# Optimization experiments

Hardware: AMD Instinct MI355X
Metric: run time of the kernel (lower is better)

## Reference

```python
import jax, jax.numpy as jnp
import numpy as np
import math

N_EMBD = 1024
N_HEADS = 16
B, T = 4, 2048

def setup_inputs() -> dict:
    key = jax.random.key(0)
    k1, k2, k3 = jax.random.split(key, 3)
    x = jax.random.normal(k1, (B, T, N_EMBD), dtype=jnp.float32)
    scale = 1.0 / math.sqrt(N_EMBD)
    W_attn = jax.random.normal(k2, (N_EMBD, 3 * N_EMBD), dtype=jnp.float32) * scale
    W_proj = jax.random.normal(k3, (N_EMBD, N_EMBD), dtype=jnp.float32) * scale
    return {"x": x, "W_attn": W_attn, "W_proj": W_proj}

def reference(x, W_attn, W_proj):
    Bb, Tt, C = x.shape
    hd = C // N_HEADS
    qkv = x @ W_attn  # [B,T,3C]
    q, k, v = jnp.split(qkv, 3, axis=-1)
    # [B,H,T,hd]
    q = q.reshape(Bb, Tt, N_HEADS, hd).transpose(0, 2, 1, 3)
    k = k.reshape(Bb, Tt, N_HEADS, hd).transpose(0, 2, 1, 3)
    v = v.reshape(Bb, Tt, N_HEADS, hd).transpose(0, 2, 1, 3)
    att = jnp.einsum('bhqd,bhkd->bhqk', q, k) * (1.0 / math.sqrt(hd))
    mask = jnp.tril(jnp.ones((Tt, Tt), dtype=bool))
    att = jnp.where(mask[None, None], att, -jnp.inf)
    att = jax.nn.softmax(att, axis=-1)
    out = jnp.einsum('bhqk,bhkd->bhqd', att, v)
    out = out.transpose(0, 2, 1, 3).reshape(Bb, Tt, C)
    return out @ W_proj
```

## Files before the change

kernel.cpp:

```cpp
#include <hip/hip_runtime.h>
#include <cstddef>
#include <cstdint>

typedef __attribute__((ext_vector_type(8))) _Float16 half8;
typedef __attribute__((ext_vector_type(4))) _Float16 half4;
typedef __attribute__((ext_vector_type(4))) float f32x4;
typedef __attribute__((ext_vector_type(16))) float f32x16;

#define N_EMBD 1024
#define N_HEADS 16
#define BATCH 4
#define SEQ 2048
#define C3 3072
#define HD 64

__device__ inline uint32_t pk2(float x, float y) {
    auto h2 = __builtin_amdgcn_cvt_pkrtz(x, y);
    uint32_t u;
    __builtin_memcpy(&u, &h2, 4);
    return u;
}

__device__ inline void swap32(uint32_t& a, uint32_t& b) {
    asm volatile("v_permlane32_swap_b32 %0, %1" : "+v"(a), "+v"(b));
}

__global__ void cvt_f32_f16(const float* __restrict__ in, _Float16* __restrict__ out, int n) {
    int i = (blockIdx.x * 256 + threadIdx.x) * 4;
    if (i >= n) return;
    float4 v = *(const float4*)(in + i);
    half4 h;
    h[0] = (_Float16)v.x; h[1] = (_Float16)v.y; h[2] = (_Float16)v.z; h[3] = (_Float16)v.w;
    *(half4*)(out + i) = h;
}

__global__ void transpose_cvt(const float* __restrict__ in, _Float16* __restrict__ out,
                              int R, int Ncols) {
    __shared__ float tile[32][33];
    int n0 = blockIdx.x * 32, r0 = blockIdx.y * 32;
    int tx = threadIdx.x, ty = threadIdx.y;
#pragma unroll
    for (int i = 0; i < 32; i += 8)
        tile[ty + i][tx] = in[(size_t)(r0 + ty + i) * Ncols + n0 + tx];
    __syncthreads();
#pragma unroll
    for (int i = 0; i < 32; i += 8)
        out[(size_t)(n0 + ty + i) * R + r0 + tx] = (_Float16)tile[tx][ty + i];
}

__global__ void transpose_v(const _Float16* __restrict__ qkv, _Float16* __restrict__ vT) {
    __shared__ _Float16 tile[32][36];
    int t0 = blockIdx.x * 32;
    int bhd = blockIdx.y;
    int bh = bhd >> 1, dh = bhd & 1;
    int b = bh >> 4, h = bh & 15;
    int tx = threadIdx.x, ty = threadIdx.y;
#pragma unroll
    for (int i = 0; i < 32; i += 8)
        tile[ty + i][tx] = qkv[(size_t)(b * SEQ + t0 + ty + i) * C3 + 2 * N_EMBD + h * HD + dh * 32 + tx];
    __syncthreads();
#pragma unroll
    for (int i = 0; i < 32; i += 8)
        vT[((size_t)bh * HD + dh * 32 + ty + i) * SEQ + t0 + tx] = tile[tx][ty + i];
}

__device__ inline void store1(float* p, float v) { *p = v; }
__device__ inline void store1(_Float16* p, float v) { *p = (_Float16)v; }

template <typename OutT>
__global__ __launch_bounds__(512, 1) void gemm192(
    const _Float16* __restrict__ A, const _Float16* __restrict__ Bt,
    OutT* __restrict__ C, int M, int N, int K) {
    __shared__ _Float16 Al[2][256 * 64];
    __shared__ _Float16 Bl[2][192 * 64];
    const int tid = threadIdx.x;
    const int lane = tid & 63, wave = tid >> 6;
    const int l15 = lane & 15, l4 = lane >> 4;
    const int wm = wave >> 2, wn = wave & 3;

    const int nwg = gridDim.x, nbx = N / 192;
    int wg = blockIdx.x;
    if ((nwg & 7) == 0) { int cpx = nwg >> 3; wg = (wg & 7) * cpx + (wg >> 3); }
    const int row0 = (wg / nbx) * 256, col0 = (wg % nbx) * 192;
    const int TAU = K >> 6;

    const int srow = tid >> 3, su = tid & 7;
    const int usrc8 = (su ^ (srow & 7)) * 8;
    auto stageAu = [&](int unit, int ts) {
        __builtin_amdgcn_global_load_lds(
            (const __attribute__((address_space(1))) void*)(A + (size_t)(row0 + unit * 64 + srow) * K + ts * 64 + usrc8),
            (__attribute__((address_space(3))) void*)(&Al[ts & 1][unit * 64 * 64 + tid * 8]), 16, 0, 0);
    };
    auto stageBu = [&](int unit, int ts) {
        __builtin_amdgcn_global_load_lds(
            (const __attribute__((address_space(1))) void*)(Bt + (size_t)(col0 + unit * 64 + srow) * K + ts * 64 + usrc8),
            (__attribute__((address_space(3))) void*)(&Bl[ts & 1][unit * 64 * 64 + tid * 8]), 16, 0, 0);
    };
    auto stageTile = [&](int ts) {
        stageAu(0, ts); stageAu(1, ts); stageAu(2, ts); stageAu(3, ts);
        stageBu(0, ts); stageBu(1, ts); stageBu(2, ts);
    };

    f32x4 acc[8][3] = {};
    stageTile(0); stageTile(1);
    asm volatile("s_waitcnt vmcnt(7)" ::: "memory");
    __builtin_amdgcn_s_barrier();

    half8 a[4][2], b[3][2];
    for (int tau = 0; tau < TAU; ++tau) {
        const _Float16* Ab = &Al[tau & 1][0];
        const _Float16* Bb = &Bl[tau & 1][0];
        const bool t2 = (tau + 2 < TAU);

#pragma unroll
        for (int m = 0; m < 4; ++m)
#pragma unroll
            for (int ks = 0; ks < 2; ++ks) {
                int r = wm * 128 + m * 16 + l15;
                a[m][ks] = *(const half8*)(Ab + r * 64 + (((ks * 4 + l4) ^ (r & 7)) * 8));
            }
#pragma unroll
        for (int n = 0; n < 3; ++n)
#pragma unroll
            for (int ks = 0; ks < 2; ++ks) {
                int r = wn * 48 + n * 16 + l15;
                b[n][ks] = *(const half8*)(Bb + r * 64 + (((ks * 4 + l4) ^ (r & 7)) * 8));
            }
        __builtin_amdgcn_s_barrier();
        __builtin_amdgcn_s_setprio(1);
#pragma unroll
        for (int m = 0; m < 4; ++m)
#pragma unroll
            for (int n = 0; n < 2; ++n)
#pragma unroll
                for (int ks = 0; ks < 2; ++ks)
                    acc[m][n] = __builtin_amdgcn_mfma_f32_16x16x32_f16(a[m][ks], b[n][ks], acc[m][n], 0, 0, 0);
        __builtin_amdgcn_s_setprio(0);
        __builtin_amdgcn_s_barrier();

        if (t2) { stageBu(0, tau + 2); stageBu(1, tau + 2); stageBu(2, tau + 2); }
        __builtin_amdgcn_s_barrier();
        __builtin_amdgcn_s_setprio(1);
#pragma unroll
        for (int m = 0; m < 4; ++m)
#pragma unroll
            for (int ks = 0; ks < 2; ++ks)
                acc[m][2] = __builtin_amdgcn_mfma_f32_16x16x32_f16(a[m][ks], b[2][ks], acc[m][2], 0, 0, 0);
        __builtin_amdgcn_s_setprio(0);
        __builtin_amdgcn_s_barrier();

#pragma unroll
        for (int m = 0; m < 4; ++m)
#pragma unroll
            for (int ks = 0; ks < 2; ++ks) {
                int r = wm * 128 + 64 + m * 16 + l15;
                a[m][ks] = *(const half8*)(Ab + r * 64 + (((ks * 4 + l4) ^ (r & 7)) * 8));
            }
        if (t2) { stageAu(0, tau + 2); stageAu(2, tau + 2); }
        __builtin_amdgcn_s_barrier();
        __builtin_amdgcn_s_setprio(1);
#pragma unroll
        for (int m = 0; m < 4; ++m)
#pragma unroll
            for (int n = 0; n < 2; ++n)
#pragma unroll
                for (int ks = 0; ks < 2; ++ks)
                    acc[4 + m][n] = __builtin_amdgcn_mfma_f32_16x16x32_f16(a[m][ks], b[n][ks], acc[4 + m][n], 0, 0, 0);
        __builtin_amdgcn_s_setprio(0);
        __builtin_amdgcn_s_barrier();

        if (t2) { stageAu(1, tau + 2); stageAu(3, tau + 2); }
        __builtin_amdgcn_s_barrier();
        __builtin_amdgcn_s_setprio(1);
#pragma unroll
        for (int m = 0; m < 4; ++m)
#pragma unroll
            for (int ks = 0; ks < 2; ++ks)
                acc[4 + m][2] = __builtin_amdgcn_mfma_f32_16x16x32_f16(a[m][ks], b[2][ks], acc[4 + m][2], 0, 0, 0);
        __builtin_amdgcn_s_setprio(0);
        if (tau <= TAU - 3) {
            asm volatile("s_waitcnt vmcnt(7)" ::: "memory");
        } else if (tau == TAU - 2) {
            asm volatile("s_waitcnt vmcnt(0)" ::: "memory");
        }
        __builtin_amdgcn_s_barrier();
    }

#pragma unroll
    for (int mi = 0; mi < 8; ++mi)
#pragma unroll
        for (int ni = 0; ni < 3; ++ni)
#pragma unroll
            for (int j = 0; j < 4; ++j) {
                int r = row0 + wm * 128 + (mi >> 2) * 64 + (mi & 3) * 16 + l4 * 4 + j;
                int c = col0 + wn * 48 + ni * 16 + l15;
                store1(C + (size_t)r * N + c, acc[mi][ni][j]);
            }
}

template <typename OutT>
__global__ __launch_bounds__(256, 2) void gemm_h(
    const _Float16* __restrict__ A, const _Float16* __restrict__ Bt,
    OutT* __restrict__ C, int M, int N, int K) {
    __shared__ _Float16 Al[3][128 * 32];
    __shared__ _Float16 Bl[3][128 * 32];
    const int tid = threadIdx.x;
    const int wave = tid >> 6, lane = tid & 63;
    const int l15 = lane & 15, l4 = lane >> 4;
    const int gx = gridDim.x;
    int lin = blockIdx.y * gx + blockIdx.x;
    int bcol, brow;
    if ((gx & 7) == 0) {
        int cpx = gx >> 3;
        int xcd = lin & 7;
        int idx = lin >> 3;
        bcol = xcd * cpx + idx % cpx;
        brow = idx / cpx;
    } else { bcol = blockIdx.x; brow = blockIdx.y; }
    const int row0 = brow * 128, col0 = bcol * 128;
    const int wm = wave >> 1, wn = wave & 1;
    const int TAU = K >> 5;

    auto stageT = [&](int ts, int buf) {
#pragma unroll
        for (int i = 0; i < 2; ++i) {
            int c = tid + 256 * i;
            int r = c >> 2, c8 = (c & 3) * 8;
            __builtin_amdgcn_global_load_lds(
                (const __attribute__((address_space(1))) void*)(A + (size_t)(row0 + r) * K + ts * 32 + c8),
                (__attribute__((address_space(3))) void*)(&Al[buf][(size_t)(wave * 64 + 256 * i) * 8]),
                16, 0, 0);
        }
#pragma unroll
        for (int i = 0; i < 2; ++i) {
            int c = tid + 256 * i;
            int r = c >> 2, c8 = (c & 3) * 8;
            __builtin_amdgcn_global_load_lds(
                (const __attribute__((address_space(1))) void*)(Bt + (size_t)(col0 + r) * K + ts * 32 + c8),
                (__attribute__((address_space(3))) void*)(&Bl[buf][(size_t)(wave * 64 + 256 * i) * 8]),
                16, 0, 0);
        }
    };

    f32x4 acc[4][4] = {};
    stageT(0, 0); stageT(1, 1);
    asm volatile("s_waitcnt vmcnt(4)" ::: "memory");
    __builtin_amdgcn_s_barrier();

    int cur = 0;
    for (int t = 0; t < TAU; ++t) {
        int sb = cur + 2; if (sb >= 3) sb -= 3;
        if (t + 2 < TAU) stageT(t + 2, sb);
        half8 a[4], b[4];
#pragma unroll
        for (int m = 0; m < 4; ++m)
            a[m] = *(const half8*)(&Al[cur][(wm * 64 + m * 16 + l15) * 32 + l4 * 8]);
#pragma unroll
        for (int n = 0; n < 4; ++n)
            b[n] = *(const half8*)(&Bl[cur][(wn * 64 + n * 16 + l15) * 32 + l4 * 8]);
        __builtin_amdgcn_s_setprio(1);
#pragma unroll
        for (int m = 0; m < 4; ++m)
#pragma unroll
            for (int n = 0; n < 4; ++n)
                acc[m][n] = __builtin_amdgcn_mfma_f32_16x16x32_f16(a[m], b[n], acc[m][n], 0, 0, 0);
        __builtin_amdgcn_s_setprio(0);
        if (t + 2 < TAU) {
            asm volatile("s_waitcnt vmcnt(4)" ::: "memory");
        } else if (t + 1 < TAU) {
            asm volatile("s_waitcnt vmcnt(0)" ::: "memory");
        }
        __builtin_amdgcn_s_barrier();
        ++cur; if (cur == 3) cur = 0;
    }
#pragma unroll
    for (int m = 0; m < 4; ++m)
#pragma unroll
        for (int n = 0; n < 4; ++n)
#pragma unroll
            for (int j = 0; j < 4; ++j) {
                int r = row0 + wm * 64 + m * 16 + l4 * 4 + j;
                int cc = col0 + wn * 64 + n * 16 + l15;
                store1(C + (size_t)r * N + cc, acc[m][n][j]);
            }
}

__global__ __launch_bounds__(256, 4) void attn_kernel(const _Float16* __restrict__ qkv,
                                                      const _Float16* __restrict__ vT,
                                                      _Float16* __restrict__ ao) {
    const int bid = blockIdx.x;
    const int qt = 15 - (bid >> 6);
    const int bh = bid & 63;
    const int b = bh >> 4, h = bh & 15;
    const int tid = threadIdx.x, lane = tid & 63;
    const int wave = tid >> 6;
    const int l31 = lane & 31, L = lane >> 5;

    __shared__ _Float16 Kl[2][64 * 64];
    __shared__ _Float16 Vl[2][64 * 64];

    const float qscale = 0.125f * 1.44269504089f;
    const float NEGC = -4.0f * 1.44269504089f;

    const int q0w = qt * 128 + wave * 32;
    const int q_g = q0w + l31;
    const int nt = 2 * qt + 2;

    auto stage = [&](int t, int buf) {
#pragma unroll
        for (int i = 0; i < 2; ++i) {
            int idx = tid + 256 * i;
            int key = idx >> 3, u = idx & 7;
            int d8 = (u ^ (key & 7)) * 8;
            __builtin_amdgcn_global_load_lds(
                (const __attribute__((address_space(1))) void*)(qkv + (size_t)(b * SEQ + t * 64 + key) * C3 + N_EMBD + h * HD + d8),
                (__attribute__((address_space(3))) void*)(&Kl[buf][idx * 8]), 16, 0, 0);
        }
#pragma unroll
        for (int i = 0; i < 2; ++i) {
            int idx = tid + 256 * i;
            int d = idx >> 3, u = idx & 7;
            int k8 = (u ^ (d & 7)) * 8;
            __builtin_amdgcn_global_load_lds(
                (const __attribute__((address_space(1))) void*)(vT + ((size_t)bh * HD + d) * SEQ + t * 64 + k8),
                (__attribute__((address_space(3))) void*)(&Vl[buf][idx * 8]), 16, 0, 0);
        }
    };

    stage(0, 0);

    half8 qb[4];
#pragma unroll
    for (int ks = 0; ks < 4; ++ks) {
        half8 v = *(const half8*)(qkv + (size_t)(b * SEQ + q_g) * C3 + h * HD + ks * 16 + L * 8);
#pragma unroll
        for (int e = 0; e < 8; ++e) v[e] = (_Float16)((float)v[e] * qscale);
        qb[ks] = v;
    }
    half8 onesf;
#pragma unroll
    for (int e = 0; e < 8; ++e) onesf[e] = (_Float16)1.0f;

    const f32x16 cinit = (f32x16)(NEGC);
    f32x16 o[2];
    o[0] = (f32x16)(0.f);
    o[1] = (f32x16)(0.f);
    f32x16 lac = (f32x16)(0.f);

    asm volatile("s_waitcnt vmcnt(0)" ::: "memory");
    __builtin_amdgcn_s_barrier();

    for (int t = 0; t < nt; ++t) {
        const int cur = t & 1;
        const int kv0 = t * 64;
        const bool pf = (t + 1 < nt);
        if (pf) stage(t + 1, cur ^ 1);

        if (kv0 <= q0w + 31) {
            const _Float16* Kb = &Kl[cur][0];
            const _Float16* Vb = &Vl[cur][0];
            f32x16 s[2];
            __builtin_amdgcn_s_setprio(1);
#pragma unroll
            for (int kb = 0; kb < 2; ++kb) {
                const int key = kb * 32 + l31;
                {
                    half8 kf = *(const half8*)(Kb + key * 64 + ((L ^ (key & 7)) * 8));
                    s[kb] = __builtin_amdgcn_mfma_f32_32x32x16_f16(kf, qb[0], cinit, 0, 0, 0);
                }
#pragma unroll
                for (int ks = 1; ks < 4; ++ks) {
                    half8 kf = *(const half8*)(Kb + key * 64 + (((ks * 2 + L) ^ (key & 7)) * 8));
                    s[kb] = __builtin_amdgcn_mfma_f32_32x32x16_f16(kf, qb[ks], s[kb], 0, 0, 0);
                }
            }
            __builtin_amdgcn_s_setprio(0);
            const bool needmask = (kv0 + 63 > q0w);
#pragma unroll
            for (int kb = 0; kb < 2; ++kb) {
#pragma unroll
                for (int r = 0; r < 16; ++r) {
                    float v = exp2f(s[kb][r]);
                    if (needmask) {
                        int key_g = kv0 + kb * 32 + (r & 3) + 8 * (r >> 2) + 4 * L;
                        v = (key_g > q_g) ? 0.f : v;
                    }
                    s[kb][r] = v;
                }
            }
            half8 paf[4];
#pragma unroll
            for (int kb = 0; kb < 2; ++kb)
#pragma unroll
                for (int hf = 0; hf < 2; ++hf) {
                    const int bse = hf * 8;
                    uint32_t a0 = pk2(s[kb][bse + 0], s[kb][bse + 1]);
                    uint32_t b0 = pk2(s[kb][bse + 4], s[kb][bse + 5]);
                    swap32(a0, b0);
                    uint32_t a1 = pk2(s[kb][bse + 2], s[kb][bse + 3]);
                    uint32_t b1 = pk2(s[kb][bse + 6], s[kb][bse + 7]);
                    swap32(a1, b1);
                    uint32_t w[4] = {a0, a1, b0, b1};
                    __builtin_memcpy(&paf[kb * 2 + hf], w, 16);
                }
            __builtin_amdgcn_s_setprio(1);
#pragma unroll
            for (int ks = 0; ks < 4; ++ks) {
                lac = __builtin_amdgcn_mfma_f32_32x32x16_f16(paf[ks], onesf, lac, 0, 0, 0);
#pragma unroll
                for (int db = 0; db < 2; ++db) {
                    const int d = db * 32 + l31;
                    half8 vb = *(const half8*)(Vb + d * 64 + (((ks * 2 + L) ^ (d & 7)) * 8));
                    o[db] = __builtin_amdgcn_mfma_f32_32x32x16_f16(paf[ks], vb, o[db], 0, 0, 0);
                }
            }
            __builtin_amdgcn_s_setprio(0);
        }

        if (pf) { asm volatile("s_waitcnt vmcnt(0)" ::: "memory"); }
        __builtin_amdgcn_s_barrier();
    }

#pragma unroll
    for (int db = 0; db < 2; ++db)
#pragma unroll
        for (int r = 0; r < 16; ++r) {
            int qg = q0w + (r & 3) + 8 * (r >> 2) + 4 * L;
            ao[(size_t)(b * SEQ + qg) * N_EMBD + h * HD + db * 32 + l31] =
                (_Float16)(o[db][r] / lac[r]);
        }
}

extern "C" void kernel_launch(void* const* d_in, const int* in_sizes, int n_in,
                              void* d_out, int out_size, void* d_ws, size_t ws_size,
                              hipStream_t stream) {
    const float* x  = (const float*)d_in[0];
    const float* Wa = (const float*)d_in[1];
    const float* Wp = (const float*)d_in[2];
    float* out = (float*)d_out;

    const int M = BATCH * SEQ;
    _Float16* xh  = (_Float16*)d_ws;
    _Float16* WaT = xh + (size_t)M * N_EMBD;
    _Float16* WpT = WaT + (size_t)C3 * N_EMBD;
    _Float16* qkv = WpT + (size_t)N_EMBD * N_EMBD;
    _Float16* ao  = qkv + (size_t)M * C3;
    _Float16* vT  = xh;

    int nx = M * N_EMBD;
    cvt_f32_f16<<<nx / 4 / 256, 256, 0, stream>>>(x, xh, nx);
    dim3 tb(32, 8);
    transpose_cvt<<<dim3(C3 / 32, N_EMBD / 32), tb, 0, stream>>>(Wa, WaT, N_EMBD, C3);
    transpose_cvt<<<dim3(N_EMBD / 32, N_EMBD / 32), tb, 0, stream>>>(Wp, WpT, N_EMBD, N_EMBD);

    gemm192<_Float16><<<dim3((M / 256) * (C3 / 192)), 512, 0, stream>>>(xh, WaT, qkv, M, C3, N_EMBD);

    transpose_v<<<dim3(SEQ / 32, BATCH * N_HEADS * 2), tb, 0, stream>>>(qkv, vT);

    attn_kernel<<<dim3(1024), 256, 0, stream>>>(qkv, vT, ao);

    gemm_h<float><<<dim3(N_EMBD / 128, M / 128), 256, 0, stream>>>(ao, WpT, out, M, N_EMBD, N_EMBD);
}
```

Before: 200.0 us.

## Triple-buffer attention K/V loads and revert GEMM to single-buffered sync loop

The attention kernel moves from double to triple buffering of K/V tiles in LDS, prefetching two tiles ahead with partial vmcnt waits. The loop body is specialised per buffer index through compile-time constants so LDS addresses fold to constants. Occupancy bounds drop from 4 to 3 blocks per CU to fit the larger shared memory. The GEMM kernel, by contrast, loses its 3-stage global-to-LDS pipeline and now loads one tile, syncs, computes, and syncs again, which exposes load latency. Unused precomputed staging indices are also added.

```diff
diff --git a/kernel.cpp b/kernel.cpp
--- a/kernel.cpp
+++ b/kernel.cpp
@@ -13,6 +13,8 @@
 #define SEQ 2048
 #define C3 3072
 #define HD 64
+
+template <int N> struct IC { static constexpr int value = N; };
 
 __device__ inline uint32_t pk2(float x, float y) {
     auto h2 = __builtin_amdgcn_cvt_pkrtz(x, y);
@@ -202,8 +204,8 @@
 __global__ __launch_bounds__(256, 2) void gemm_h(
     const _Float16* __restrict__ A, const _Float16* __restrict__ Bt,
     OutT* __restrict__ C, int M, int N, int K) {
-    __shared__ _Float16 Al[3][128 * 32];
-    __shared__ _Float16 Bl[3][128 * 32];
+    __shared__ _Float16 Al[128 * 32];
+    __shared__ _Float16 Bl[128 * 32];
     const int tid = threadIdx.x;
     const int wave = tid >> 6, lane = tid & 63;
     const int l15 = lane & 15, l4 = lane >> 4;
@@ -219,16 +221,15 @@
     } else { bcol = blockIdx.x; brow = blockIdx.y; }
     const int row0 = brow * 128, col0 = bcol * 128;
     const int wm = wave >> 1, wn = wave & 1;
-    const int TAU = K >> 5;
-
-    auto stageT = [&](int ts, int buf) {
+    f32x4 acc[4][4] = {};
+    for (int k0 = 0; k0 < K; k0 += 32) {
 #pragma unroll
         for (int i = 0; i < 2; ++i) {
             int c = tid + 256 * i;
             int r = c >> 2, c8 = (c & 3) * 8;
             __builtin_amdgcn_global_load_lds(
-                (const __attribute__((address_space(1))) void*)(A + (size_t)(row0 + r) * K + ts * 32 + c8),
-                (__attribute__((address_space(3))) void*)(&Al[buf][(size_t)(wave * 64 + 256 * i) * 8]),
+                (const __attribute__((address_space(1))) void*)(A + (size_t)(row0 + r) * K + k0 + c8),
+                (__attribute__((address_space(3))) void*)(Al + (size_t)(wave * 64 + 256 * i) * 8),
                 16, 0, 0);
         }
 #pragma unroll
@@ -236,28 +237,18 @@
             int c = tid + 256 * i;
             int r = c >> 2, c8 = (c & 3) * 8;
             __builtin_amdgcn_global_load_lds(
-                (const __attribute__((address_space(1))) void*)(Bt + (size_t)(col0 + r) * K + ts * 32 + c8),
-                (__attribute__((address_space(3))) void*)(&Bl[buf][(size_t)(wave * 64 + 256 * i) * 8]),
+                (const __attribute__((address_space(1))) void*)(Bt + (size_t)(col0 + r) * K + k0 + c8),
+                (__attribute__((address_space(3))) void*)(Bl + (size_t)(wave * 64 + 256 * i) * 8),
                 16, 0, 0);
         }
-    };
-
-    f32x4 acc[4][4] = {};
-    stageT(0, 0); stageT(1, 1);
-    asm volatile("s_waitcnt vmcnt(4)" ::: "memory");
-    __builtin_amdgcn_s_barrier();
-
-    int cur = 0;
-    for (int t = 0; t < TAU; ++t) {
-        int sb = cur + 2; if (sb >= 3) sb -= 3;
-        if (t + 2 < TAU) stageT(t + 2, sb);
+        __syncthreads();
         half8 a[4], b[4];
 #pragma unroll
         for (int m = 0; m < 4; ++m)
-            a[m] = *(const half8*)(&Al[cur][(wm * 64 + m * 16 + l15) * 32 + l4 * 8]);
+            a[m] = *(const half8*)(Al + (wm * 64 + m * 16 + l15) * 32 + l4 * 8);
 #pragma unroll
         for (int n = 0; n < 4; ++n)
-            b[n] = *(const half8*)(&Bl[cur][(wn * 64 + n * 16 + l15) * 32 + l4 * 8]);
+            b[n] = *(const half8*)(Bl + (wn * 64 + n * 16 + l15) * 32 + l4 * 8);
         __builtin_amdgcn_s_setprio(1);
 #pragma unroll
         for (int m = 0; m < 4; ++m)
@@ -265,13 +256,7 @@
             for (int n = 0; n < 4; ++n)
                 acc[m][n] = __builtin_amdgcn_mfma_f32_16x16x32_f16(a[m], b[n], acc[m][n], 0, 0, 0);
         __builtin_amdgcn_s_setprio(0);
-        if (t + 2 < TAU) {
-            asm volatile("s_waitcnt vmcnt(4)" ::: "memory");
-        } else if (t + 1 < TAU) {
-            asm volatile("s_waitcnt vmcnt(0)" ::: "memory");
-        }
-        __builtin_amdgcn_s_barrier();
-        ++cur; if (cur == 3) cur = 0;
+        __syncthreads();
     }
 #pragma unroll
     for (int m = 0; m < 4; ++m)
@@ -285,7 +270,7 @@
             }
 }
 
-__global__ __launch_bounds__(256, 4) void attn_kernel(const _Float16* __restrict__ qkv,
+__global__ __launch_bounds__(256, 3) void attn_kernel(const _Float16* __restrict__ qkv,
                                                       const _Float16* __restrict__ vT,
                                                       _Float16* __restrict__ ao) {
     const int bid = blockIdx.x;
@@ -296,8 +281,8 @@
     const int wave = tid >> 6;
     const int l31 = lane & 31, L = lane >> 5;
 
-    __shared__ _Float16 Kl[2][64 * 64];
-    __shared__ _Float16 Vl[2][64 * 64];
+    __shared__ _Float16 Kl[3][64 * 64];
+    __shared__ _Float16 Vl[3][64 * 64];
 
     const float qscale = 0.125f * 1.44269504089f;
     const float NEGC = -4.0f * 1.44269504089f;
@@ -306,28 +291,35 @@
     const int q_g = q0w + l31;
     const int nt = 2 * qt + 2;
 
-    auto stage = [&](int t, int buf) {
+    const int sk_key = tid >> 3, sk_u = tid & 7;
+    const int sk_d8 = (sk_u ^ (sk_key & 7)) * 8;
+    const int sv_d = tid >> 3;
+    const int sv_k8 = (sk_u ^ (sv_d & 7)) * 8;
+
+    auto stage = [&](int t, auto bufc) {
+        constexpr int BUF = decltype(bufc)::value;
 #pragma unroll
         for (int i = 0; i < 2; ++i) {
             int idx = tid + 256 * i;
-            int key = idx >> 3, u = idx & 7;
-            int d8 = (u ^ (key & 7)) * 8;
+            int key = idx >> 3;
+            int d8 = ((idx & 7) ^ (key & 7)) * 8;
             __builtin_amdgcn_global_load_lds(
                 (const __attribute__((address_space(1))) void*)(qkv + (size_t)(b * SEQ + t * 64 + key) * C3 + N_EMBD + h * HD + d8),
-                (__attribute__((address_space(3))) void*)(&Kl[buf][idx * 8]), 16, 0, 0);
+                (__attribute__((address_space(3))) void*)(&Kl[BUF][idx * 8]), 16, 0, 0);
         }
 #pragma unroll
         for (int i = 0; i < 2; ++i) {
             int idx = tid + 256 * i;
-            int d = idx >> 3, u = idx & 7;
-            int k8 = (u ^ (d & 7)) * 8;
+            int d = idx >> 3;
+            int k8 = ((idx & 7) ^ (d & 7)) * 8;
             __builtin_amdgcn_global_load_lds(
                 (const __attribute__((address_space(1))) void*)(vT + ((size_t)bh * HD + d) * SEQ + t * 64 + k8),
-                (__attribute__((address_space(3))) void*)(&Vl[buf][idx * 8]), 16, 0, 0);
+                (__attribute__((address_space(3))) void*)(&Vl[BUF][idx * 8]), 16, 0, 0);
         }
     };
 
-    stage(0, 0);
+    stage(0, IC<0>{});
+    stage(1, IC<1>{});
 
     half8 qb[4];
 #pragma unroll
@@ -347,78 +339,87 @@
     o[1] = (f32x16)(0.f);
     f32x16 lac = (f32x16)(0.f);
 
-    asm volatile("s_waitcnt vmcnt(0)" ::: "memory");
+    asm volatile("s_waitcnt vmcnt(4)" ::: "memory");
     __builtin_amdgcn_s_barrier();
 
+    int c3 = 0;
     for (int t = 0; t < nt; ++t) {
-        const int cur = t & 1;
-        const int kv0 = t * 64;
-        const bool pf = (t + 1 < nt);
-        if (pf) stage(t + 1, cur ^ 1);
-
-        if (kv0 <= q0w + 31) {
-            const _Float16* Kb = &Kl[cur][0];
-            const _Float16* Vb = &Vl[cur][0];
-            f32x16 s[2];
-            __builtin_amdgcn_s_setprio(1);
-#pragma unroll
-            for (int kb = 0; kb < 2; ++kb) {
-                const int key = kb * 32 + l31;
-                {
-                    half8 kf = *(const half8*)(Kb + key * 64 + ((L ^ (key & 7)) * 8));
-                    s[kb] = __builtin_amdgcn_mfma_f32_32x32x16_f16(kf, qb[0], cinit, 0, 0, 0);
+        auto step = [&](auto curc) {
+            constexpr int CUR = decltype(curc)::value;
+            constexpr int SB = (CUR + 2) % 3;
+            const int kv0 = t * 64;
+            if (t + 2 < nt) stage(t + 2, IC<SB>{});
+
+            if (kv0 <= q0w + 31) {
+                f32x16 s[2];
+                __builtin_amdgcn_s_setprio(1);
+#pragma unroll
+                for (int kb = 0; kb < 2; ++kb) {
+                    const int key = kb * 32 + l31;
+                    {
+                        half8 kf = *(const half8*)(&Kl[CUR][key * 64 + ((L ^ (key & 7)) * 8)]);
+                        s[kb] = __builtin_amdgcn_mfma_f32_32x32x16_f16(kf, qb[0], cinit, 0, 0, 0);
+                    }
+#pragma unroll
+                    for (int ks = 1; ks < 4; ++ks) {
+                        half8 kf = *(const half8*)(&Kl[CUR][key * 64 + (((ks * 2 + L) ^ (key & 7)) * 8)]);
+                        s[kb] = __builtin_amdgcn_mfma_f32_32x32x16_f16(kf, qb[ks], s[kb], 0, 0, 0);
+                    }
                 }
-#pragma unroll
-                for (int ks = 1; ks < 4; ++ks) {
-                    half8 kf = *(const half8*)(Kb + key * 64 + (((ks * 2 + L) ^ (key & 7)) * 8));
-                    s[kb] = __builtin_amdgcn_mfma_f32_32x32x16_f16(kf, qb[ks], s[kb], 0, 0, 0);
+                __builtin_amdgcn_s_setprio(0);
+                const bool needmask = (kv0 + 63 > q0w);
+#pragma unroll
+                for (int kb = 0; kb < 2; ++kb) {
+#pragma unroll
+                    for (int r = 0; r < 16; ++r) {
+                        float v = exp2f(s[kb][r]);
+                        if (needmask) {
+                            int key_g = kv0 + kb * 32 + (r & 3) + 8 * (r >> 2) + 4 * L;
+                            v = (key_g > q_g) ? 0.f : v;
+                        }
+                        s[kb][r] = v;
+                    }
                 }
-            }
-            __builtin_amdgcn_s_setprio(0);
-            const bool needmask = (kv0 + 63 > q0w);
-#pragma unroll
-            for (int kb = 0; kb < 2; ++kb) {
-#pragma unroll
-                for (int r = 0; r < 16; ++r) {
-                    float v = exp2f(s[kb][r]);
-                    if (needmask) {
-                        int key_g = kv0 + kb * 32 + (r & 3) + 8 * (r >> 2) + 4 * L;
-                        v = (key_g > q_g) ? 0.f : v;
+                half8 paf[4];
+#pragma unroll
+                for (int kb = 0; kb < 2; ++kb)
+#pragma unroll
+                    for (int hf = 0; hf < 2; ++hf) {
+                        const int bse = hf * 8;
+                        uint32_t a0 = pk2(s[kb][bse + 0], s[kb][bse + 1]);
+                        uint32_t b0 = pk2(s[kb][bse + 4], s[kb][bse + 5]);
+                        swap32(a0, b0);
+                        uint32_t a1 = pk2(s[kb][bse + 2], s[kb][bse + 3]);
+                        uint32_t b1 = pk2(s[kb][bse + 6], s[kb][bse + 7]);
+                        swap32(a1, b1);
+                        uint32_t w[4] = {a0, a1, b0, b1};
+                        __builtin_memcpy(&paf[kb * 2 + hf], w, 16);
                     }
-                    s[kb][r] = v;
+                __builtin_amdgcn_s_setprio(1);
+#pragma unroll
+                for (int ks = 0; ks < 4; ++ks) {
+                    lac = __builtin_amdgcn_mfma_f32_32x32x16_f16(paf[ks], onesf, lac, 0, 0, 0);
+#pragma unroll
+                    for (int db = 0; db < 2; ++db) {
+                        const int d = db * 32 + l31;
+                        half8 vb = *(const half8*)(&Vl[CUR][d * 64 + (((ks * 2 + L) ^ (d & 7)) * 8)]);
+                        o[db] = __builtin_amdgcn_mfma_f32_32x32x16_f16(paf[ks], vb, o[db], 0, 0, 0);
+                    }
                 }
-            }
-            half8 paf[4];
-#pragma unroll
-            for (int kb = 0; kb < 2; ++kb)
-#pragma unroll
-                for (int hf = 0; hf < 2; ++hf) {
-                    const int bse = hf * 8;
-                    uint32_t a0 = pk2(s[kb][bse + 0], s[kb][bse + 1]);
-                    uint32_t b0 = pk2(s[kb][bse + 4], s[kb][bse + 5]);
-                    swap32(a0, b0);
-                    uint32_t a1 = pk2(s[kb][bse + 2], s[kb][bse + 3]);
-                    uint32_t b1 = pk2(s[kb][bse + 6], s[kb][bse + 7]);
-                    swap32(a1, b1);
-                    uint32_t w[4] = {a0, a1, b0, b1};
-                    __builtin_memcpy(&paf[kb * 2 + hf], w, 16);
-                }
-            __builtin_amdgcn_s_setprio(1);
-#pragma unroll
-            for (int ks = 0; ks < 4; ++ks) {
-                lac = __builtin_amdgcn_mfma_f32_32x32x16_f16(paf[ks], onesf, lac, 0, 0, 0);
-#pragma unroll
-                for (int db = 0; db < 2; ++db) {
-                    const int d = db * 32 + l31;
-                    half8 vb = *(const half8*)(Vb + d * 64 + (((ks * 2 + L) ^ (d & 7)) * 8));
-                    o[db] = __builtin_amdgcn_mfma_f32_32x32x16_f16(paf[ks], vb, o[db], 0, 0, 0);
-                }
-            }
-            __builtin_amdgcn_s_setprio(0);
-        }
-
-        if (pf) { asm volatile("s_waitcnt vmcnt(0)" ::: "memory"); }
-        __builtin_amdgcn_s_barrier();
+                __builtin_amdgcn_s_setprio(0);
+            }
+
+            if (t + 2 < nt) {
+                asm volatile("s_waitcnt vmcnt(4)" ::: "memory");
+            } else if (t + 1 < nt) {
+                asm volatile("s_waitcnt vmcnt(0)" ::: "memory");
+            }
+            __builtin_amdgcn_s_barrier();
+        };
+        if (c3 == 0) step(IC<0>{});
+        else if (c3 == 1) step(IC<1>{});
+        else step(IC<2>{});
+        ++c3; if (c3 == 3) c3 = 0;
     }
 
 #pragma unroll
```

Result: slower. 262.3 us (+31.2%).
